# Optimization experiments

Measured on AMD Instinct MI355X. Metric: run time of the kernel, lower is better.

The kernel has to match this reference:

```python
import jax, jax.numpy as jnp
import numpy as np

B, S, D, H = 8, 384, 768, 12
MAX_POS = 512
P = 2 * MAX_POS - 1  # 1023


def setup_inputs() -> dict:
    key = jax.random.key(0)
    ks = jax.random.split(key, 14)
    w = 0.02
    return {
        "x": jax.random.normal(ks[0], (B, S, D), jnp.float32),
        "rel_pos_emb": jax.random.normal(ks[1], (P, D), jnp.float32),
        "Wq": jax.random.normal(ks[2], (D, D), jnp.float32) * w,
        "bq": jax.random.normal(ks[3], (D,), jnp.float32) * w,
        "Wk": jax.random.normal(ks[4], (D, D), jnp.float32) * w,
        "bk": jax.random.normal(ks[5], (D,), jnp.float32) * w,
        "Wv": jax.random.normal(ks[6], (D, D), jnp.float32) * w,
        "bv": jax.random.normal(ks[7], (D,), jnp.float32) * w,
        "q_bias": jax.random.normal(ks[8], (D,), jnp.float32) * w,
        "v_bias": jax.random.normal(ks[9], (D,), jnp.float32) * w,
        "Wpk": jax.random.normal(ks[10], (D, D), jnp.float32) * w,
        "Wpq": jax.random.normal(ks[11], (D, D), jnp.float32) * w,
        "Wo": jax.random.normal(ks[12], (D, D), jnp.float32) * w,
        "bo": jax.random.normal(ks[13], (D,), jnp.float32) * w,
    }


def reference(x, rel_pos_emb, Wq, bq, Wk, bk, Wv, bv, q_bias, v_bias, Wpk, Wpq, Wo, bo):
    b, s, d = x.shape
    dh = d // H
    scale = dh ** -0.5
    # relative position index: rel[i, j] = j - i + MAX_POS - 1
    rel = (jnp.arange(s)[None, :] - jnp.arange(s)[:, None]) + MAX_POS - 1
    emb = rel_pos_emb[rel]                      # [S, S, D]
    q = (x @ Wq + bq + q_bias).reshape(b, s, H, dh)
    k = (x @ Wk + bk).reshape(b, s, H, dh)
    v = (x @ Wv + bv + v_bias).reshape(b, s, H, dh)
    Kp = (emb @ Wpk).reshape(s, s, H, dh)       # pos keys   [i, j, h, d]
    Qp = (emb @ Wpq).reshape(s, s, H, dh)       # pos queries[i, j, h, d]
    c2c = jnp.einsum('bihd,bjhd->bhij', q, k)
    c2p = jnp.einsum('bihd,ijhd->bhij', q, Kp)
    p2c = jnp.einsum('ijhd,bjhd->bhij', Qp, k)
    scores = (c2c + c2p + p2c) * scale          # [B, H, S, S]
    w = jax.nn.softmax(scores, axis=-1)
    out = jnp.einsum('bhij,bjhd->bihd', w, v).reshape(b, s, d)
    return out @ Wo + bo
```

## Files before the change

kernel.cpp:

```cpp
#include <hip/hip_runtime.h>
#include <hip/hip_bf16.h>
#include <math.h>

#define BATCH 8
#define SEQ 384
#define DIM 768
#define NH 12
#define DH 64
#define NPOS 767
#define POS_OFF 128
#define NTOK (BATCH * SEQ)
#define QKN 1536
#define QKVN 2304
#define PN 1536

typedef __attribute__((ext_vector_type(8))) short short8;
typedef __attribute__((ext_vector_type(4))) float floatx4;
typedef unsigned int u32;

__device__ __forceinline__ ushort f2bf(float f) {
    __hip_bfloat16 h = __float2bfloat16(f);
    return *reinterpret_cast<ushort*>(&h);
}
__device__ __forceinline__ float bf2f(ushort u) {
    u32 x = ((u32)u) << 16;
    float f; __builtin_memcpy(&f, &x, 4); return f;
}

__device__ __forceinline__ void gld16(const ushort* g, ushort* l) {
    __builtin_amdgcn_global_load_lds(
        (const __attribute__((address_space(1))) u32*)g,
        (__attribute__((address_space(3))) u32*)l, 16, 0, 0);
}

#define MFMA __builtin_amdgcn_mfma_f32_16x16x32_bf16

__global__ __launch_bounds__(256) void prep(
    const float* W0, const float* W1, const float* W2,
    const float* W3, const float* W4, const float* W5,
    const float* x, const float* rpe,
    ushort* __restrict__ wsT, ushort* __restrict__ xb, ushort* __restrict__ rpeb)
{
    const int tid = threadIdx.x;
    if (blockIdx.z < 6) {
        __shared__ float t[64][65];
        const float* srcs[6] = {W0, W1, W2, W3, W4, W5};
        const float* in = srcs[blockIdx.z];
        ushort* out = wsT + (size_t)blockIdx.z * DIM * DIM;
        const int r0 = blockIdx.y * 64, c0 = blockIdx.x * 64;
        for (int p = 0; p < 16; ++p) {
            int e = tid + p * 256, i = e >> 6, j = e & 63;
            t[i][j] = in[(size_t)(r0 + i) * DIM + c0 + j];
        }
        __syncthreads();
        for (int p = 0; p < 16; ++p) {
            int e = tid + p * 256, i = e >> 6, j = e & 63;
            out[(size_t)(c0 + i) * DIM + r0 + j] = f2bf(t[j][i]);
        }
    } else {
        const int n4x = NTOK * DIM / 4;
        const int n4p = NPOS * DIM / 4;
        const int fb = blockIdx.y * 12 + blockIdx.x;
        for (int idx = fb * 256 + tid; idx < n4x + n4p; idx += 144 * 256) {
            const float* src; ushort* dst; int j;
            if (idx < n4x) { src = x; dst = xb; j = idx; }
            else { src = rpe + (size_t)POS_OFF * DIM; dst = rpeb; j = idx - n4x; }
            float4 f = ((const float4*)src)[j];
            ushort o[4] = {f2bf(f.x), f2bf(f.y), f2bf(f.z), f2bf(f.w)};
            *(uint2*)&dst[(size_t)j * 4] = *(uint2*)o;
        }
    }
}

__global__ __launch_bounds__(256) void proj_all(
    const ushort* __restrict__ xb, const ushort* __restrict__ rpeb,
    const ushort* __restrict__ wsT,
    const float* __restrict__ bq, const float* __restrict__ qbias,
    const float* __restrict__ bk, const float* __restrict__ bv,
    const float* __restrict__ vbias,
    ushort* __restrict__ qk, ushort* __restrict__ vT, ushort* __restrict__ posKQ)
{
    __shared__ ushort As[128 * 64];
    __shared__ ushort Bs[128 * 64];
    const int tid = threadIdx.x;
    const int lane = tid & 63, w = tid >> 6;
    const int id = blockIdx.x;
    const bool qkvP = id < 432;
    const ushort* A; const ushort* Bt; int m0, n0, M;
    if (qkvP) {
        m0 = (id % 24) * 128; n0 = (id / 24) * 128;
        A = xb; Bt = wsT; M = NTOK;
    } else {
        int p = id - 432;
        m0 = (p % 6) * 128; n0 = (p / 6) * 128;
        A = rpeb; Bt = wsT + (size_t)3 * DIM * DIM; M = NPOS;
    }
    const int lr = lane >> 3;
    const int lc = (lane & 7) ^ (lr & 7);
    const ushort* ga[4]; const ushort* gb[4];
#pragma unroll
    for (int p = 0; p < 4; ++p) {
        int row = (w * 4 + p) * 8 + lr;
        int arow = m0 + row; if (arow > M - 1) arow = M - 1;
        ga[p] = A + (size_t)arow * DIM + lc * 8;
        gb[p] = Bt + (size_t)(n0 + row) * DIM + lc * 8;
    }
    floatx4 acc[4][4] = {};
    const int qr = (w >> 1) * 64, qc = (w & 1) * 64;
    const int lm = lane & 15, lk = lane >> 4;
    for (int k0 = 0; k0 < DIM; k0 += 64) {
#pragma unroll
        for (int p = 0; p < 4; ++p) {
            gld16(ga[p], As + (w * 4 + p) * 512);
            gld16(gb[p], Bs + (w * 4 + p) * 512);
            ga[p] += 64; gb[p] += 64;
        }
        __syncthreads();
#pragma unroll
        for (int kk = 0; kk < 2; ++kk) {
            int ch = (kk * 4 + lk) ^ (lm & 7);
            short8 af[4], bf[4];
#pragma unroll
            for (int t = 0; t < 4; ++t) {
                af[t] = *(const short8*)&As[(qr + t * 16 + lm) * 64 + ch * 8];
                bf[t] = *(const short8*)&Bs[(qc + t * 16 + lm) * 64 + ch * 8];
            }
#pragma unroll
            for (int i = 0; i < 4; ++i)
#pragma unroll
                for (int j = 0; j < 4; ++j)
                    acc[i][j] = MFMA(af[i], bf[j], acc[i][j], 0, 0, 0);
        }
        __syncthreads();
    }
    if (qkvP) {
#pragma unroll
        for (int i = 0; i < 4; ++i) {
            int mbase = m0 + qr + i * 16 + (lane >> 4) * 4;
            int bb = mbase / SEQ;
            int s0 = mbase - bb * SEQ;
#pragma unroll
            for (int j = 0; j < 4; ++j) {
                int n = n0 + qc + j * 16 + lm;
                float bs;
                if (n < 768) bs = bq[n] + qbias[n];
                else if (n < QKN) bs = bk[n - 768];
                else bs = bv[n - QKN] + vbias[n - QKN];
                if (n < QKN) {
#pragma unroll
                    for (int r = 0; r < 4; ++r)
                        qk[(size_t)(mbase + r) * QKN + n] = f2bf(acc[i][j][r] + bs);
                } else {
                    int c = n - QKN, h = c >> 6, d = c & 63;
                    ushort tmp[4];
#pragma unroll
                    for (int r = 0; r < 4; ++r) tmp[r] = f2bf(acc[i][j][r] + bs);
                    *(uint2*)&vT[(((size_t)bb * NH + h) * DH + d) * SEQ + s0] = *(uint2*)tmp;
                }
            }
        }
    } else {
#pragma unroll
        for (int i = 0; i < 4; ++i) {
            int mbase = m0 + qr + i * 16 + (lane >> 4) * 4;
#pragma unroll
            for (int j = 0; j < 4; ++j) {
                int n = n0 + qc + j * 16 + lm;
#pragma unroll
                for (int r = 0; r < 4; ++r) {
                    int row = mbase + r;
                    if (row < NPOS)
                        posKQ[(size_t)row * PN + n] = f2bf(acc[i][j][r]);
                }
            }
        }
    }
}

__global__ __launch_bounds__(256) void gemm128x64(
    const ushort* __restrict__ A, const ushort* __restrict__ Bt,
    const float* __restrict__ bias, float* __restrict__ outF,
    int M, int N, int K)
{
    __shared__ ushort As[128 * 64];
    __shared__ ushort Bs[64 * 64];
    const int tid = threadIdx.x;
    const int lane = tid & 63, w = tid >> 6;
    const int n0 = blockIdx.x * 64, m0 = blockIdx.y * 128;
    const int lr = lane >> 3;
    const int lc = (lane & 7) ^ (lr & 7);
    const ushort* ga[4]; const ushort* gb[2];
#pragma unroll
    for (int p = 0; p < 4; ++p) {
        int arow = m0 + (w * 4 + p) * 8 + lr; if (arow > M - 1) arow = M - 1;
        ga[p] = A + (size_t)arow * K + lc * 8;
    }
#pragma unroll
    for (int p = 0; p < 2; ++p)
        gb[p] = Bt + (size_t)(n0 + (w * 2 + p) * 8 + lr) * K + lc * 8;
    floatx4 acc[4][2] = {};
    const int qr = (w >> 1) * 64, qc = (w & 1) * 32;
    const int lm = lane & 15, lk = lane >> 4;
    for (int k0 = 0; k0 < K; k0 += 64) {
#pragma unroll
        for (int p = 0; p < 4; ++p) { gld16(ga[p], As + (w * 4 + p) * 512); ga[p] += 64; }
#pragma unroll
        for (int p = 0; p < 2; ++p) { gld16(gb[p], Bs + (w * 2 + p) * 512); gb[p] += 64; }
        __syncthreads();
#pragma unroll
        for (int kk = 0; kk < 2; ++kk) {
            int ch = (kk * 4 + lk) ^ (lm & 7);
            short8 af[4], bf[2];
#pragma unroll
            for (int t = 0; t < 4; ++t)
                af[t] = *(const short8*)&As[(qr + t * 16 + lm) * 64 + ch * 8];
#pragma unroll
            for (int t = 0; t < 2; ++t)
                bf[t] = *(const short8*)&Bs[(qc + t * 16 + lm) * 64 + ch * 8];
#pragma unroll
            for (int i = 0; i < 4; ++i)
#pragma unroll
                for (int j = 0; j < 2; ++j)
                    acc[i][j] = MFMA(af[i], bf[j], acc[i][j], 0, 0, 0);
        }
        __syncthreads();
    }
#pragma unroll
    for (int i = 0; i < 4; ++i) {
        int mbase = m0 + qr + i * 16 + (lane >> 4) * 4;
#pragma unroll
        for (int j = 0; j < 2; ++j) {
            int n = n0 + qc + j * 16 + lm;
            float bs = bias[n];
#pragma unroll
            for (int r = 0; r < 4; ++r) {
                int row = mbase + r;
                if (row < M) outF[(size_t)row * N + n] = acc[i][j][r] + bs;
            }
        }
    }
}

__global__ __launch_bounds__(512, 2) void attn_fused15(
    const ushort* __restrict__ qk, const ushort* __restrict__ vT,
    const ushort* __restrict__ posKQ, ushort* __restrict__ aob)
{
    __shared__ ushort kt[64 * 64];
    __shared__ ushort kps[128 * 64];
    __shared__ ushort cc[64 * 72];
    __shared__ ushort dqs[64 * 72];
    __shared__ ushort dks[64 * 72];

    const int tid = threadIdx.x;
    const int lane = tid & 63, w = tid >> 6;
    const int i0 = blockIdx.x * 64;
    const int h = blockIdx.y, b = blockIdx.z;
    const int lm = lane & 15, lq = lane >> 4;
    const int lr = lane >> 3, l8 = lane & 7;
    const int lc = l8 ^ (lr & 7);

    short8 qf[2];
    {
        const ushort* qr = qk + (size_t)(b * SEQ + i0 + (w >> 1) * 16 + lm) * QKN + h * DH;
        qf[0] = *(const short8*)(qr + lq * 8);
        qf[1] = *(const short8*)(qr + 32 + lq * 8);
    }
    const ushort* kb = qk + 768 + h * DH;
    floatx4 occ[2] = {};
    float rs = 0.f;

    const int t0i = 320 - i0;
    const int tcb = (w & 1) * 4;
    const int tr = w >> 1;

    {
        gld16(kb + (size_t)(b * SEQ + 8 * w + lr) * QKN + lc * 8, kt + w * 512);
        gld16(posKQ + (size_t)(t0i + 16 * w + lr) * PN + h * DH + lc * 8, kps + w * 1024);
        gld16(posKQ + (size_t)(t0i + 16 * w + 8 + lr) * PN + h * DH + lc * 8, kps + w * 1024 + 512);
    }

    for (int jt = 0; jt < 6; ++jt) {
        const int j0 = jt * 64;
        __syncthreads();

        short8 qpf[2];
        {
            const ushort* qpb = posKQ + (size_t)(t0i + j0 + w * 16 + lm) * PN
                                + 768 + h * DH + lq * 8;
            qpf[0] = *(const short8*)(qpb);
            qpf[1] = *(const short8*)(qpb + 32);
        }

        {
            int tjb = (w & 1) * 2;
            floatx4 a0 = {}, a1 = {};
#pragma unroll
            for (int kk = 0; kk < 2; ++kk) {
                int ch = (kk * 4 + lq) ^ (lm & 7);
                short8 b0 = *(const short8*)&kt[(tjb * 16 + lm) * 64 + ch * 8];
                short8 b1 = *(const short8*)&kt[((tjb + 1) * 16 + lm) * 64 + ch * 8];
                a0 = MFMA(qf[kk], b0, a0, 0, 0, 0);
                a1 = MFMA(qf[kk], b1, a1, 0, 0, 0);
            }
#pragma unroll
            for (int r = 0; r < 4; ++r) {
                cc[(tr * 16 + lq * 4 + r) * 72 + tjb * 16 + lm] = f2bf(a0[r]);
                cc[(tr * 16 + lq * 4 + r) * 72 + (tjb + 1) * 16 + lm] = f2bf(a1[r]);
            }
        }
        {
            floatx4 d[4] = {};
#pragma unroll
            for (int kk = 0; kk < 2; ++kk) {
                int ch = (kk * 4 + lq) ^ (lm & 7);
#pragma unroll
                for (int s = 0; s < 4; ++s) {
                    short8 bf = *(const short8*)&kps[((tcb + s) * 16 + lm) * 64 + ch * 8];
                    d[s] = MFMA(qf[kk], bf, d[s], 0, 0, 0);
                }
            }
#pragma unroll
            for (int s = 0; s < 4; ++s) {
                int t = (tcb + s) * 16 + lm;
#pragma unroll
                for (int r = 0; r < 4; ++r) {
                    int i = tr * 16 + lq * 4 + r;
                    int j = t + i - 63;
                    if ((unsigned)j < 64u) dqs[i * 72 + j] = f2bf(d[s][r]);
                }
            }
        }
        {
            floatx4 e[4] = {};
#pragma unroll
            for (int kk = 0; kk < 2; ++kk) {
                int ch = (kk * 4 + lq) ^ (lm & 7);
#pragma unroll
                for (int s = 0; s < 4; ++s) {
                    short8 bf = *(const short8*)&kt[(s * 16 + lm) * 64 + ch * 8];
                    e[s] = MFMA(qpf[kk], bf, e[s], 0, 0, 0);
                }
            }
#pragma unroll
            for (int s = 0; s < 4; ++s) {
                int j = s * 16 + lm;
#pragma unroll
                for (int r = 0; r < 4; ++r) {
                    int t = w * 16 + lq * 4 + r;
                    int i = j - t + 63;
                    if ((unsigned)i < 64u) dks[i * 72 + j] = f2bf(e[s][r]);
                }
            }
        }
        __syncthreads();

        if (jt < 5) {
            int t0n = t0i + j0 + 64;
            gld16(kb + (size_t)(b * SEQ + j0 + 64 + 8 * w + lr) * QKN + lc * 8, kt + w * 512);
            gld16(posKQ + (size_t)(t0n + 16 * w + lr) * PN + h * DH + lc * 8, kps + w * 1024);
            gld16(posKQ + (size_t)(t0n + 16 * w + 8 + lr) * PN + h * DH + lc * 8, kps + w * 1024 + 512);
        }

        {
            const int off = (tr * 16 + lm) * 72 + lq * 8;
            short8 af0, af1;
            float psum = 0.f;
            {
                uint4 c4 = *(const uint4*)&cc[off];
                uint4 q4 = *(const uint4*)&dqs[off];
                uint4 k4 = *(const uint4*)&dks[off];
                const ushort* cu = (const ushort*)&c4;
                const ushort* qu = (const ushort*)&q4;
                const ushort* ku = (const ushort*)&k4;
                ushort pv[8];
#pragma unroll
                for (int c = 0; c < 8; ++c) {
                    float pe = __expf((bf2f(cu[c]) + bf2f(qu[c]) + bf2f(ku[c])) * 0.125f);
                    psum += pe;
                    pv[c] = f2bf(pe);
                }
                af0 = *(const short8*)pv;
            }
            {
                uint4 c4 = *(const uint4*)&cc[off + 32];
                uint4 q4 = *(const uint4*)&dqs[off + 32];
                uint4 k4 = *(const uint4*)&dks[off + 32];
                const ushort* cu = (const ushort*)&c4;
                const ushort* qu = (const ushort*)&q4;
                const ushort* ku = (const ushort*)&k4;
                ushort pv[8];
#pragma unroll
                for (int c = 0; c < 8; ++c) {
                    float pe = __expf((bf2f(cu[c]) + bf2f(qu[c]) + bf2f(ku[c])) * 0.125f);
                    psum += pe;
                    pv[c] = f2bf(pe);
                }
                af1 = *(const short8*)pv;
            }
            psum += __shfl_xor(psum, 16);
            psum += __shfl_xor(psum, 32);
            rs += psum;

            int dtb = (w & 1) * 2;
#pragma unroll
            for (int t2 = 0; t2 < 2; ++t2) {
                int dt = dtb + t2;
                const ushort* vr = vT + ((size_t)(b * NH + h) * DH + dt * 16 + lm) * SEQ + j0;
                short8 vf0 = *(const short8*)(vr + lq * 8);
                short8 vf1 = *(const short8*)(vr + 32 + lq * 8);
                occ[t2] = MFMA(af0, vf0, occ[t2], 0, 0, 0);
                occ[t2] = MFMA(af1, vf1, occ[t2], 0, 0, 0);
            }
        }
    }

    {
        int dtb = (w & 1) * 2;
#pragma unroll
        for (int t2 = 0; t2 < 2; ++t2) {
#pragma unroll
            for (int r = 0; r < 4; ++r) {
                int row = tr * 16 + lq * 4 + r;
                float rsv = __shfl(rs, lq * 4 + r);
                float ov = occ[t2][r] / rsv;
                aob[(size_t)(b * SEQ + i0 + row) * DIM + h * DH + (dtb + t2) * 16 + lm] = f2bf(ov);
            }
        }
    }
}

extern "C" void kernel_launch(void* const* d_in, const int* in_sizes, int n_in,
                              void* d_out, int out_size, void* d_ws, size_t ws_size,
                              hipStream_t stream) {
    const float* x   = (const float*)d_in[0];
    const float* rpe = (const float*)d_in[1];
    const float* Wq  = (const float*)d_in[2];
    const float* bq  = (const float*)d_in[3];
    const float* Wk  = (const float*)d_in[4];
    const float* bk  = (const float*)d_in[5];
    const float* Wv  = (const float*)d_in[6];
    const float* bv  = (const float*)d_in[7];
    const float* qbias = (const float*)d_in[8];
    const float* vbias = (const float*)d_in[9];
    const float* Wpk = (const float*)d_in[10];
    const float* Wpq = (const float*)d_in[11];
    const float* Wo  = (const float*)d_in[12];
    const float* bo  = (const float*)d_in[13];
    float* out = (float*)d_out;

    char* ws = (char*)d_ws;
    ushort* xb    = (ushort*)ws; ws += (size_t)NTOK * DIM * 2;
    ushort* qkbuf = (ushort*)ws; ws += (size_t)NTOK * QKN * 2;
    ushort* vT    = (ushort*)ws; ws += (size_t)NTOK * DIM * 2;
    ushort* aob   = (ushort*)ws; ws += (size_t)NTOK * DIM * 2;
    ushort* rpeb  = (ushort*)ws; ws += (size_t)NPOS * DIM * 2;
    ushort* posKQ = (ushort*)ws; ws += (size_t)NPOS * PN * 2;
    ushort* wsT   = (ushort*)ws; ws += (size_t)6 * DIM * DIM * 2;

    prep<<<dim3(12, 12, 7), dim3(256), 0, stream>>>(
        Wq, Wk, Wv, Wpk, Wpq, Wo, x, rpe, wsT, xb, rpeb);
    proj_all<<<dim3(504), dim3(256), 0, stream>>>(
        xb, rpeb, wsT, bq, qbias, bk, bv, vbias, qkbuf, vT, posKQ);
    attn_fused15<<<dim3(SEQ / 64, NH, BATCH), dim3(512), 0, stream>>>(qkbuf, vT, posKQ, aob);
    gemm128x64<<<dim3(DIM / 64, NTOK / 128), dim3(256), 0, stream>>>(
        aob, wsT + (size_t)5 * DIM * DIM, bo, out, NTOK, DIM, DIM);
}
```

Measured before the change: 183.4 us.

## Double-buffer K and positional tiles in attention and remap blocks across XCDs

The attention kernel now keeps two LDS buffers for the K and positional-key tiles. The next tile's loads are issued at the start of each iteration, so they overlap the current tile's score MFMAs instead of the softmax/PV phase. The grid is flattened to 576 blocks with an index remap, likely so blocks sharing a head are placed together on the same XCD for L2 reuse. LDS use per block grows by roughly 24 KB, which may reduce occupancy under the 2-blocks-per-CU bound.

```diff
diff --git a/kernel.cpp b/kernel.cpp
--- a/kernel.cpp
+++ b/kernel.cpp
@@ -241,20 +241,24 @@
     }
 }
 
-__global__ __launch_bounds__(512, 2) void attn_fused15(
+__global__ __launch_bounds__(512, 2) void attn_fused16(
     const ushort* __restrict__ qk, const ushort* __restrict__ vT,
     const ushort* __restrict__ posKQ, ushort* __restrict__ aob)
 {
-    __shared__ ushort kt[64 * 64];
-    __shared__ ushort kps[128 * 64];
+    __shared__ ushort kt[2][64 * 64];
+    __shared__ ushort kps[2][128 * 64];
     __shared__ ushort cc[64 * 72];
     __shared__ ushort dqs[64 * 72];
     __shared__ ushort dks[64 * 72];
 
     const int tid = threadIdx.x;
     const int lane = tid & 63, w = tid >> 6;
-    const int i0 = blockIdx.x * 64;
-    const int h = blockIdx.y, b = blockIdx.z;
+    const int m = blockIdx.x;
+    const int n = (m & 7) * 72 + (m >> 3);
+    const int h = n / 48;
+    const int rem = n - h * 48;
+    const int b = rem / 6;
+    const int i0 = (rem % 6) * 64;
     const int lm = lane & 15, lq = lane >> 4;
     const int lr = lane >> 3, l8 = lane & 7;
     const int lc = l8 ^ (lr & 7);
@@ -274,14 +278,22 @@
     const int tr = w >> 1;
 
     {
-        gld16(kb + (size_t)(b * SEQ + 8 * w + lr) * QKN + lc * 8, kt + w * 512);
-        gld16(posKQ + (size_t)(t0i + 16 * w + lr) * PN + h * DH + lc * 8, kps + w * 1024);
-        gld16(posKQ + (size_t)(t0i + 16 * w + 8 + lr) * PN + h * DH + lc * 8, kps + w * 1024 + 512);
+        gld16(kb + (size_t)(b * SEQ + 8 * w + lr) * QKN + lc * 8, kt[0] + w * 512);
+        gld16(posKQ + (size_t)(t0i + 16 * w + lr) * PN + h * DH + lc * 8, kps[0] + w * 1024);
+        gld16(posKQ + (size_t)(t0i + 16 * w + 8 + lr) * PN + h * DH + lc * 8, kps[0] + w * 1024 + 512);
     }
 
     for (int jt = 0; jt < 6; ++jt) {
         const int j0 = jt * 64;
-        __syncthreads();
+        const int cur = jt & 1, nxt = cur ^ 1;
+        __syncthreads();
+
+        if (jt < 5) {
+            int t0n = t0i + j0 + 64;
+            gld16(kb + (size_t)(b * SEQ + j0 + 64 + 8 * w + lr) * QKN + lc * 8, kt[nxt] + w * 512);
+            gld16(posKQ + (size_t)(t0n + 16 * w + lr) * PN + h * DH + lc * 8, kps[nxt] + w * 1024);
+            gld16(posKQ + (size_t)(t0n + 16 * w + 8 + lr) * PN + h * DH + lc * 8, kps[nxt] + w * 1024 + 512);
+        }
 
         short8 qpf[2];
         {
@@ -297,8 +309,8 @@
 #pragma unroll
             for (int kk = 0; kk < 2; ++kk) {
                 int ch = (kk * 4 + lq) ^ (lm & 7);
-                short8 b0 = *(const short8*)&kt[(tjb * 16 + lm) * 64 + ch * 8];
-                short8 b1 = *(const short8*)&kt[((tjb + 1) * 16 + lm) * 64 + ch * 8];
+                short8 b0 = *(const short8*)&kt[cur][(tjb * 16 + lm) * 64 + ch * 8];
+                short8 b1 = *(const short8*)&kt[cur][((tjb + 1) * 16 + lm) * 64 + ch * 8];
                 a0 = MFMA(qf[kk], b0, a0, 0, 0, 0);
                 a1 = MFMA(qf[kk], b1, a1, 0, 0, 0);
             }
@@ -315,7 +327,7 @@
                 int ch = (kk * 4 + lq) ^ (lm & 7);
 #pragma unroll
                 for (int s = 0; s < 4; ++s) {
-                    short8 bf = *(const short8*)&kps[((tcb + s) * 16 + lm) * 64 + ch * 8];
+                    short8 bf = *(const short8*)&kps[cur][((tcb + s) * 16 + lm) * 64 + ch * 8];
                     d[s] = MFMA(qf[kk], bf, d[s], 0, 0, 0);
                 }
             }
@@ -337,7 +349,7 @@
                 int ch = (kk * 4 + lq) ^ (lm & 7);
 #pragma unroll
                 for (int s = 0; s < 4; ++s) {
-                    short8 bf = *(const short8*)&kt[(s * 16 + lm) * 64 + ch * 8];
+                    short8 bf = *(const short8*)&kt[cur][(s * 16 + lm) * 64 + ch * 8];
                     e[s] = MFMA(qpf[kk], bf, e[s], 0, 0, 0);
                 }
             }
@@ -353,13 +365,6 @@
             }
         }
         __syncthreads();
-
-        if (jt < 5) {
-            int t0n = t0i + j0 + 64;
-            gld16(kb + (size_t)(b * SEQ + j0 + 64 + 8 * w + lr) * QKN + lc * 8, kt + w * 512);
-            gld16(posKQ + (size_t)(t0n + 16 * w + lr) * PN + h * DH + lc * 8, kps + w * 1024);
-            gld16(posKQ + (size_t)(t0n + 16 * w + 8 + lr) * PN + h * DH + lc * 8, kps + w * 1024 + 512);
-        }
 
         {
             const int off = (tr * 16 + lm) * 72 + lq * 8;
@@ -461,7 +466,7 @@
         Wq, Wk, Wv, Wpk, Wpq, Wo, x, rpe, wsT, xb, rpeb);
     proj_all<<<dim3(504), dim3(256), 0, stream>>>(
         xb, rpeb, wsT, bq, qbias, bk, bv, vbias, qkbuf, vT, posKQ);
-    attn_fused15<<<dim3(SEQ / 64, NH, BATCH), dim3(512), 0, stream>>>(qkbuf, vT, posKQ, aob);
+    attn_fused16<<<dim3(576), dim3(512), 0, stream>>>(qkbuf, vT, posKQ, aob);
     gemm128x64<<<dim3(DIM / 64, NTOK / 128), dim3(256), 0, stream>>>(
         aob, wsT + (size_t)5 * DIM * DIM, bo, out, NTOK, DIM, DIM);
 }
```

Measured after the change: 185.1 us. No clear change (+0.9%).
